# Kernel tuning notes

Hardware: AMD Instinct MI355X
Metric: run time of the kernel (lower is better)

The kernel has to match this reference:

```python
import jax, jax.numpy as jnp
import numpy as np

N = 50000      # nodes
IN = 128       # in_channels
H = 2          # heads
C = 64         # hidden_channels (per head)
E = 800000     # edges (before self-loops)
OUT = 40       # out_channels
BN_EPS = 1e-5
NEG_SLOPE = 0.2  # PyG GATConv default


def _bn(x, g, b):
    # BatchNorm1d forward with batch statistics (training-mode math, biased var)
    mu = jnp.mean(x, axis=0)
    v = jnp.var(x, axis=0)
    return (x - mu) * jax.lax.rsqrt(v + BN_EPS) * g + b


def _gat_conv(x, src, dst, W, a_src, a_dst, bias, concat):
    n = x.shape[0]
    h = (x @ W).reshape(n, H, C)                      # [N,H,C] per-head projection
    al_s = jnp.einsum('nhc,hc->nh', h, a_src)         # [N,H]
    al_d = jnp.einsum('nhc,hc->nh', h, a_dst)
    e = jax.nn.leaky_relu(al_s[src] + al_d[dst], NEG_SLOPE)  # [E,H]
    # segment softmax over edges sharing the same destination
    m = jax.ops.segment_max(e, dst, num_segments=n)
    ex = jnp.exp(e - m[dst])
    s = jax.ops.segment_sum(ex, dst, num_segments=n)
    alpha = ex / s[dst]                               # [E,H]
    out = jax.ops.segment_sum(h[src] * alpha[..., None], dst, num_segments=n)  # [N,H,C]
    out = out.reshape(n, H * C) if concat else out.mean(axis=1)
    return out + bias


def setup_inputs() -> dict:
    key = jax.random.key(0)
    ks = jax.random.split(key, 16)
    g = lambda k, shp, scale=1.0: jax.random.normal(k, shp, dtype=jnp.float32) * scale
    x = g(ks[0], (N, IN))
    edge_index = jax.random.randint(ks[1], (2, E), 0, N, dtype=jnp.int32)
    s = 1.0 / np.sqrt(IN)
    s2 = 1.0 / np.sqrt(H * C)
    return {
        'x': x,
        'edge_index': edge_index,
        'bn0_g': jnp.ones((IN,), jnp.float32), 'bn0_b': jnp.zeros((IN,), jnp.float32),
        'W1': g(ks[2], (IN, H * C), s), 'a1_src': g(ks[3], (H, C), s), 'a1_dst': g(ks[4], (H, C), s),
        'b1': jnp.zeros((H * C,), jnp.float32),
        'bn1_g': jnp.ones((H * C,), jnp.float32), 'bn1_b': jnp.zeros((H * C,), jnp.float32),
        'W2': g(ks[5], (H * C, H * C), s2), 'a2_src': g(ks[6], (H, C), s2), 'a2_dst': g(ks[7], (H, C), s2),
        'b2': jnp.zeros((C,), jnp.float32),
        'bn2_g': jnp.ones((C,), jnp.float32), 'bn2_b': jnp.zeros((C,), jnp.float32),
        'Wf': g(ks[8], (C, OUT), 1.0 / np.sqrt(C)), 'bf': jnp.zeros((OUT,), jnp.float32),
    }


def reference(x, edge_index, bn0_g, bn0_b, W1, a1_src, a1_dst, b1, bn1_g, bn1_b,
              W2, a2_src, a2_dst, b2, bn2_g, bn2_b, Wf, bf):
    n = x.shape[0]
    loop = jnp.arange(n, dtype=edge_index.dtype)
    src = jnp.concatenate([edge_index[0], loop])  # add self-loops (PyG default)
    dst = jnp.concatenate([edge_index[1], loop])
    h = _bn(x, bn0_g, bn0_b)
    # layer 1: concat heads
    h = _gat_conv(h, src, dst, W1, a1_src, a1_dst, b1, concat=True)
    h = jax.nn.elu(_bn(h, bn1_g, bn1_b))
    # (dropout is identity in eval mode)
    # layer 2: average heads
    h = _gat_conv(h, src, dst, W2, a2_src, a2_dst, b2, concat=False)
    h = jax.nn.elu(_bn(h, bn2_g, bn2_b))
    return h @ Wf + bf
```

## Files before the change

### kernel.cpp

```cpp
#include <hip/hip_runtime.h>
#include <hip/hip_fp16.h>


#define NEG_SLOPE 0.2f
#define BN_EPS 1e-5f

typedef short bf16x8 __attribute__((ext_vector_type(8)));
typedef float f32x4 __attribute__((ext_vector_type(4)));

static __device__ __forceinline__ unsigned short f2bf(float f) {
    union { float f; unsigned u; } v; v.f = f;
    unsigned r = v.u + 0x7FFF + ((v.u >> 16) & 1);
    return (unsigned short)(r >> 16);
}
static __device__ __forceinline__ float2 bf2x2(unsigned v) {
    union { unsigned u; float f; } a, b;
    a.u = v << 16; b.u = v & 0xffff0000u;
    return make_float2(a.f, b.f);
}
static __device__ __forceinline__ float halfsel(unsigned p, int head) {
    __half2 h = *(__half2*)&p;
    return head ? __high2float(h) : __low2float(h);
}

template <int C>
static __device__ __forceinline__ void d_bnstat(const float* __restrict__ x, int M,
                                                int rowsPerBlock, float* __restrict__ sums,
                                                int b) {
    constexpr int TPR = C / 4;
    constexpr int RS  = 256 / TPR;
    __shared__ float red[4][2 * C];
    const int t = threadIdx.x;
    const int cg = t % TPR, rg = t / TPR, w = t >> 6, lane = t & 63;
    int r0 = b * rowsPerBlock + rg;
    int r1 = min(M, b * rowsPerBlock + rowsPerBlock);
    float4 s = make_float4(0, 0, 0, 0), q = make_float4(0, 0, 0, 0);
    #pragma unroll 4
    for (int r = r0; r < r1; r += RS) {
        float4 v = *(const float4*)&x[(size_t)r * C + cg * 4];
        s.x += v.x; s.y += v.y; s.z += v.z; s.w += v.w;
        q.x += v.x * v.x; q.y += v.y * v.y; q.z += v.z * v.z; q.w += v.w * v.w;
    }
    #pragma unroll
    for (int off = TPR; off < 64; off <<= 1) {
        s.x += __shfl_xor(s.x, off); s.y += __shfl_xor(s.y, off);
        s.z += __shfl_xor(s.z, off); s.w += __shfl_xor(s.w, off);
        q.x += __shfl_xor(q.x, off); q.y += __shfl_xor(q.y, off);
        q.z += __shfl_xor(q.z, off); q.w += __shfl_xor(q.w, off);
    }
    if (lane < TPR) {
        *(float4*)&red[w][cg * 4] = s;
        *(float4*)&red[w][C + cg * 4] = q;
    }
    __syncthreads();
    for (int idx = t; idx < 2 * C; idx += 256) {
        float tot = red[0][idx] + red[1][idx] + red[2][idx] + red[3][idx];
        atomicAdd(&sums[idx], tot);
    }
}

template <int C>
__global__ __launch_bounds__(256) void k_bnstat2(const float* __restrict__ x, int M,
                                                 int rowsPerBlock, float* __restrict__ sums) {
    d_bnstat<C>(x, M, rowsPerBlock, sums, blockIdx.x);
}

__global__ __launch_bounds__(256) void k_prep(
    const int* __restrict__ ei, int E, int S, int NR,
    const float* __restrict__ x, int M, int bgrid,
    const float* __restrict__ W1, const float* __restrict__ W2,
    unsigned short* __restrict__ cnt, unsigned short* __restrict__ rank,
    float* __restrict__ sums,
    unsigned short* __restrict__ wt1, unsigned short* __restrict__ wt2) {
    int b = blockIdx.x;
    int CG = 8 * S;
    if (b < CG) {
        __shared__ unsigned lcnt[8192];
        const int t = threadIdx.x;
        const int r = b & 7, s = b >> 3;
        const unsigned lo = (unsigned)(r * NR);
        for (int j = t; j < NR; j += 256) lcnt[j] = 0;
        __syncthreads();
        int i1 = min(E, (s + 1) << 15);
        for (int i = (s << 15) + t; i < i1; i += 256) {
            unsigned d = (unsigned)ei[E + i];
            unsigned rel = d - lo;
            if (rel < (unsigned)NR) {
                unsigned old = atomicAdd(&lcnt[rel], 1u);
                rank[i] = (unsigned short)old;
            }
        }
        __syncthreads();
        for (int j = t; j < NR; j += 256) {
            int node = (int)lo + j;
            if (node < M) cnt[(size_t)s * M + node] = (unsigned short)lcnt[j];
        }
    } else if (b < CG + bgrid) {
        d_bnstat<128>(x, M, 256, sums, b - CG);
    } else {
        int idx = (b - CG - bgrid) * 256 + threadIdx.x;
        if (idx < 128 * 128) {
            int n = idx >> 7, k = idx & 127;
            wt1[idx] = f2bf(W1[k * 128 + n]);
            wt2[idx] = f2bf(W2[k * 128 + n]);
        }
    }
}

__global__ __launch_bounds__(1024) void k_part(const unsigned short* __restrict__ cnt,
                                               int Nn, int S, int* __restrict__ part) {
    __shared__ int ws[16];
    int t = threadIdx.x, lane = t & 63, w = t >> 6;
    int i = blockIdx.x * 1024 + t;
    int v = 0;
    if (i < Nn) {
        for (int s = 0; s < S; s++) v += (int)cnt[(size_t)s * Nn + i];
        v += 1;
    }
    #pragma unroll
    for (int off = 32; off; off >>= 1) v += __shfl_xor(v, off);
    if (lane == 0) ws[w] = v;
    __syncthreads();
    if (t < 16) {
        int s = ws[t];
        #pragma unroll
        for (int off = 8; off; off >>= 1) s += __shfl_xor(s, off);
        if (t == 0) part[blockIdx.x] = s;
    }
}

__global__ __launch_bounds__(1024) void k_scan2(unsigned short* __restrict__ cnt,
                                                int Nn, int S, int nb,
                                                const int* __restrict__ part,
                                                int* __restrict__ rowptr) {
    __shared__ int wsum[16];
    __shared__ int s_base, s_total;
    int t = threadIdx.x, lane = t & 63, w = t >> 6;
    int b = blockIdx.x;
    if (w == 0) {
        int base = 0, total = 0;
        for (int ch = 0; ch < nb; ch += 64) {
            int j = ch + lane;
            int v = (j < nb) ? part[j] : 0;
            total += v;
            base += (j < b) ? v : 0;
        }
        #pragma unroll
        for (int off = 32; off; off >>= 1) {
            base += __shfl_xor(base, off);
            total += __shfl_xor(total, off);
        }
        if (lane == 0) { s_base = base; s_total = total; }
    }
    int i = b * 1024 + t;
    int v = 0;
    if (i < Nn) {
        int run = 0;
        for (int s = 0; s < S; s++) {
            int cv = (int)cnt[(size_t)s * Nn + i];
            cnt[(size_t)s * Nn + i] = (unsigned short)run;
            run += cv;
        }
        v = run + 1;
    }
    int x = v;
    #pragma unroll
    for (int off = 1; off < 64; off <<= 1) {
        int y = __shfl_up(x, off);
        if (lane >= off) x += y;
    }
    if (lane == 63) wsum[w] = x;
    __syncthreads();
    if (w == 0) {
        int val = (lane < 16) ? wsum[lane] : 0;
        int xs = val;
        #pragma unroll
        for (int off = 1; off < 16; off <<= 1) {
            int y = __shfl_up(xs, off);
            if (lane >= off) xs += y;
        }
        if (lane < 16) wsum[lane] = xs - val;
    }
    __syncthreads();
    if (i < Nn) rowptr[i] = s_base + wsum[w] + (x - v);
    if (b == nb - 1 && t == 0) rowptr[Nn] = s_total;
}

static __device__ __forceinline__ void d_fill(int b, const int* __restrict__ ei,
                                              const unsigned short* __restrict__ rank,
                                              const unsigned short* __restrict__ pofs,
                                              const int* __restrict__ rowptr, int E, int Nn,
                                              unsigned short* __restrict__ ssrc) {
    int i = b * 256 + threadIdx.x;
    if (i < E) {
        int s = ei[i], d = ei[E + i];
        int p = i >> 15;
        int rk = (int)pofs[(size_t)p * Nn + d] + (int)rank[i];
        ssrc[rowptr[d] + 1 + rk] = (unsigned short)s;
    } else if (i < E + Nn) {
        int d = i - E;
        ssrc[rowptr[d]] = (unsigned short)d;
    }
}

static __device__ __forceinline__ void d_mfma(
    int blk, const float* __restrict__ A, const unsigned short* __restrict__ wt,
    const float* __restrict__ sums, const float* __restrict__ bng, const float* __restrict__ bnb,
    int elu, const float* __restrict__ asrc, const float* __restrict__ adst, int M,
    unsigned short* __restrict__ hb, float* __restrict__ als, float* __restrict__ ald) {
    __shared__ unsigned short As[64 * 136];
    __shared__ unsigned short Bs[128 * 136];
    __shared__ __align__(16) float stl[256];
    const int t = threadIdx.x;
    const int w = t >> 6, lane = t & 63;
    const int c = lane & 15, q = lane >> 4;
    const int row0 = blk * 64;

    if (t < 128) {
        float mu = sums[t] / (float)M;
        float var = sums[128 + t] / (float)M - mu * mu;
        float s = bng[t] * rsqrtf(var + BN_EPS);
        stl[t] = s;
        stl[128 + t] = bnb[t] - mu * s;
    }
    __syncthreads();

    #pragma unroll
    for (int i = 0; i < 8; i++) {
        int idx = t + i * 256;
        int r = idx >> 5, ch4 = idx & 31;
        int gr = row0 + r;
        float4 v = make_float4(0, 0, 0, 0);
        if (gr < M) {
            v = *(const float4*)&A[(size_t)gr * 128 + ch4 * 4];
            float4 sc = *(const float4*)&stl[ch4 * 4];
            float4 sh = *(const float4*)&stl[128 + ch4 * 4];
            v.x = v.x * sc.x + sh.x; v.y = v.y * sc.y + sh.y;
            v.z = v.z * sc.z + sh.z; v.w = v.w * sc.w + sh.w;
            if (elu) {
                v.x = v.x > 0.f ? v.x : expm1f(v.x);
                v.y = v.y > 0.f ? v.y : expm1f(v.y);
                v.z = v.z > 0.f ? v.z : expm1f(v.z);
                v.w = v.w > 0.f ? v.w : expm1f(v.w);
            }
        }
        unsigned p0 = ((unsigned)f2bf(v.y) << 16) | f2bf(v.x);
        unsigned p1 = ((unsigned)f2bf(v.w) << 16) | f2bf(v.z);
        *(uint2*)&As[r * 136 + ch4 * 4] = make_uint2(p0, p1);
    }
    #pragma unroll
    for (int i = 0; i < 8; i++) {
        int idx = t + i * 256;
        int r = idx >> 4, ch = idx & 15;
        *(uint4*)&Bs[r * 136 + ch * 8] = *(const uint4*)&wt[(size_t)r * 128 + ch * 8];
    }
    __syncthreads();

    f32x4 acc[8] = {};
    #pragma unroll
    for (int ks = 0; ks < 4; ks++) {
        bf16x8 a = *(bf16x8*)&As[(w * 16 + c) * 136 + (ks * 4 + q) * 8];
        #pragma unroll
        for (int tl = 0; tl < 8; tl++) {
            bf16x8 b = *(bf16x8*)&Bs[(tl * 16 + c) * 136 + (ks * 4 + q) * 8];
            acc[tl] = __builtin_amdgcn_mfma_f32_16x16x32_bf16(a, b, acc[tl], 0, 0, 0);
        }
    }

    #pragma unroll
    for (int reg = 0; reg < 4; reg++) {
        int grow = row0 + w * 16 + q * 4 + reg;
        if (grow < M) {
            #pragma unroll
            for (int tl = 0; tl < 8; tl++)
                hb[(size_t)grow * 128 + tl * 16 + c] = f2bf(acc[tl][reg]);
        }
    }

    float as_[8], ad_[8];
    #pragma unroll
    for (int tl = 0; tl < 8; tl++) { as_[tl] = asrc[tl * 16 + c]; ad_[tl] = adst[tl * 16 + c]; }
    #pragma unroll
    for (int reg = 0; reg < 4; reg++) {
        float s0 = 0.f, s1 = 0.f, d0 = 0.f, d1 = 0.f;
        #pragma unroll
        for (int tl = 0; tl < 4; tl++) { s0 += acc[tl][reg] * as_[tl]; d0 += acc[tl][reg] * ad_[tl]; }
        #pragma unroll
        for (int tl = 4; tl < 8; tl++) { s1 += acc[tl][reg] * as_[tl]; d1 += acc[tl][reg] * ad_[tl]; }
        #pragma unroll
        for (int off = 1; off < 16; off <<= 1) {
            s0 += __shfl_xor(s0, off); s1 += __shfl_xor(s1, off);
            d0 += __shfl_xor(d0, off); d1 += __shfl_xor(d1, off);
        }
        int grow = row0 + w * 16 + q * 4 + reg;
        if (c == 0 && grow < M) {
            *(float2*)&als[(size_t)grow * 2] = make_float2(s0, s1);
            *(float2*)&ald[(size_t)grow * 2] = make_float2(d0, d1);
        }
    }
}

__global__ __launch_bounds__(256) void k_mfma(
    const float* __restrict__ A, const unsigned short* __restrict__ wt,
    const float* __restrict__ sums, const float* __restrict__ bng, const float* __restrict__ bnb,
    int elu, const float* __restrict__ asrc, const float* __restrict__ adst, int M,
    unsigned short* __restrict__ hb, float* __restrict__ als, float* __restrict__ ald) {
    d_mfma(blockIdx.x, A, wt, sums, bng, bnb, elu, asrc, adst, M, hb, als, ald);
}

__global__ __launch_bounds__(256) void k_fill_mfma(
    const float* __restrict__ A, const unsigned short* __restrict__ wt,
    const float* __restrict__ sums, const float* __restrict__ bng, const float* __restrict__ bnb,
    const float* __restrict__ asrc, const float* __restrict__ adst, int M, int ggrid,
    unsigned short* __restrict__ hb, float* __restrict__ als, float* __restrict__ ald,
    const int* __restrict__ ei, const unsigned short* __restrict__ rank,
    const unsigned short* __restrict__ pofs,
    const int* __restrict__ rowptr, int E, int Nn, unsigned short* __restrict__ ssrc) {
    if (blockIdx.x < ggrid)
        d_mfma(blockIdx.x, A, wt, sums, bng, bnb, 0, asrc, adst, M, hb, als, ald);
    else
        d_fill(blockIdx.x - ggrid, ei, rank, pofs, rowptr, E, Nn, ssrc);
}

static __device__ __forceinline__ void acc8(float* acc, uint4 v, float a) {
    float2 p;
    p = bf2x2(v.x); acc[0] += a * p.x; acc[1] += a * p.y;
    p = bf2x2(v.y); acc[2] += a * p.x; acc[3] += a * p.y;
    p = bf2x2(v.z); acc[4] += a * p.x; acc[5] += a * p.y;
    p = bf2x2(v.w); acc[6] += a * p.x; acc[7] += a * p.y;
}

template <int MEAN>
static __device__ __forceinline__ void attnagg(
    const int* __restrict__ rowptr, const unsigned short* __restrict__ ssrc,
    const float* __restrict__ als, const float* __restrict__ ald,
    float* __restrict__ alpha, const unsigned short* __restrict__ hb,
    const float* __restrict__ bias, int Nn, float* __restrict__ out) {
    int gw = (blockIdx.x * blockDim.x + threadIdx.x) >> 6;
    if (gw >= Nn) return;
    int lane = threadIdx.x & 63;
    int sub = lane >> 4, c = lane & 15, head = c >> 3;
    int beg = rowptr[gw], end = rowptr[gw + 1];
    int deg = end - beg;
    float2 dv = *(const float2*)&ald[(size_t)gw * 2];
    float acc[8] = {};

    if (deg <= 64) {
        bool on = lane < deg;
        int eidx = beg + (on ? lane : 0);
        int sreg = (int)ssrc[eidx];
        float2 av = *(const float2*)&als[(size_t)sreg * 2];
        float v0 = av.x + dv.x; v0 = v0 > 0.f ? v0 : NEG_SLOPE * v0;
        float v1 = av.y + dv.y; v1 = v1 > 0.f ? v1 : NEG_SLOPE * v1;
        float p0 = on ? __expf(v0) : 0.f;
        float p1 = on ? __expf(v1) : 0.f;
        float t0 = p0, t1 = p1;
        #pragma unroll
        for (int off = 32; off; off >>= 1) {
            t0 += __shfl_xor(t0, off);
            t1 += __shfl_xor(t1, off);
        }
        __half2 hpk = __floats2half2_rn(p0 / t0, p1 / t1);
        unsigned pk = *(unsigned*)&hpk;

        int nit = (deg + 3) >> 2;
        int it = 0;
        for (; it + 4 <= nit; it += 4) {
            int s_[4]; float a_[4];
            #pragma unroll
            for (int u = 0; u < 4; u++) {
                int jj = (it + u) * 4 + sub;
                int ls = jj & 63;
                s_[u] = __shfl(sreg, ls);
                unsigned pw = (unsigned)__shfl(pk, ls);
                a_[u] = (jj < deg) ? halfsel(pw, head) : 0.f;
            }
            #pragma unroll
            for (int u = 0; u < 4; u++) {
                uint4 v = *(const uint4*)&hb[(size_t)s_[u] * 128 + c * 8];
                acc8(acc, v, a_[u]);
            }
        }
        for (; it < nit; it += 2) {
            const bool two = (it + 1) < nit;
            int s_[2]; float a_[2];
            #pragma unroll
            for (int u = 0; u < 2; u++) {
                if (u == 0 || two) {
                    int jj = (it + u) * 4 + sub;
                    int ls = jj & 63;
                    s_[u] = __shfl(sreg, ls);
                    unsigned pw = (unsigned)__shfl(pk, ls);
                    a_[u] = (jj < deg) ? halfsel(pw, head) : 0.f;
                }
            }
            #pragma unroll
            for (int u = 0; u < 2; u++) {
                if (u == 0 || two) {
                    uint4 v = *(const uint4*)&hb[(size_t)s_[u] * 128 + c * 8];
                    acc8(acc, v, a_[u]);
                }
            }
        }
    } else {
        float d0 = dv.x, d1 = dv.y;
        float m0 = -1e30f, m1 = -1e30f;
        for (int e = beg + lane; e < end; e += 64) {
            int s = (int)ssrc[e];
            float v0 = als[s * 2] + d0;     v0 = v0 > 0.f ? v0 : NEG_SLOPE * v0;
            float v1 = als[s * 2 + 1] + d1; v1 = v1 > 0.f ? v1 : NEG_SLOPE * v1;
            m0 = fmaxf(m0, v0); m1 = fmaxf(m1, v1);
        }
        #pragma unroll
        for (int off = 32; off; off >>= 1) {
            m0 = fmaxf(m0, __shfl_xor(m0, off));
            m1 = fmaxf(m1, __shfl_xor(m1, off));
        }
        float t0 = 0.f, t1 = 0.f;
        for (int e = beg + lane; e < end; e += 64) {
            int s = (int)ssrc[e];
            float v0 = als[s * 2] + d0;     v0 = v0 > 0.f ? v0 : NEG_SLOPE * v0;
            float v1 = als[s * 2 + 1] + d1; v1 = v1 > 0.f ? v1 : NEG_SLOPE * v1;
            float p0 = __expf(v0 - m0), p1 = __expf(v1 - m1);
            alpha[e * 2] = p0; alpha[e * 2 + 1] = p1;
            t0 += p0; t1 += p1;
        }
        #pragma unroll
        for (int off = 32; off; off >>= 1) {
            t0 += __shfl_xor(t0, off);
            t1 += __shfl_xor(t1, off);
        }
        float i0 = 1.f / t0, i1 = 1.f / t1;
        for (int e = beg + sub; e < end; e += 4) {
            int s = (int)ssrc[e];
            float a = (head ? alpha[(size_t)e * 2 + 1] * i1 : alpha[(size_t)e * 2] * i0);
            uint4 v = *(const uint4*)&hb[(size_t)s * 128 + c * 8];
            acc8(acc, v, a);
        }
    }

    #pragma unroll
    for (int j2 = 0; j2 < 8; j2++) {
        acc[j2] += __shfl_xor(acc[j2], 16);
        acc[j2] += __shfl_xor(acc[j2], 32);
        if (MEAN) acc[j2] += __shfl_xor(acc[j2], 8);
    }
    if (MEAN) {
        if (sub == 0 && c < 8) {
            float4 b0 = *(const float4*)&bias[c * 8];
            float4 b1 = *(const float4*)&bias[c * 8 + 4];
            float4 o0 = make_float4(0.5f * acc[0] + b0.x, 0.5f * acc[1] + b0.y, 0.5f * acc[2] + b0.z, 0.5f * acc[3] + b0.w);
            float4 o1 = make_float4(0.5f * acc[4] + b1.x, 0.5f * acc[5] + b1.y, 0.5f * acc[6] + b1.z, 0.5f * acc[7] + b1.w);
            *(float4*)&out[(size_t)gw * 64 + c * 8] = o0;
            *(float4*)&out[(size_t)gw * 64 + c * 8 + 4] = o1;
        }
    } else {
        if (sub == 0) {
            float4 b0 = *(const float4*)&bias[c * 8];
            float4 b1 = *(const float4*)&bias[c * 8 + 4];
            float4 o0 = make_float4(acc[0] + b0.x, acc[1] + b0.y, acc[2] + b0.z, acc[3] + b0.w);
            float4 o1 = make_float4(acc[4] + b1.x, acc[5] + b1.y, acc[6] + b1.z, acc[7] + b1.w);
            *(float4*)&out[(size_t)gw * 128 + c * 8] = o0;
            *(float4*)&out[(size_t)gw * 128 + c * 8 + 4] = o1;
        }
    }
}

__global__ __launch_bounds__(256) void k_attnagg1(const int* __restrict__ rowptr, const unsigned short* __restrict__ ssrc,
                                                  const float* __restrict__ als, const float* __restrict__ ald,
                                                  float* __restrict__ alpha, const unsigned short* __restrict__ hb,
                                                  const float* __restrict__ bias, int Nn, float* __restrict__ out) {
    attnagg<0>(rowptr, ssrc, als, ald, alpha, hb, bias, Nn, out);
}

__global__ __launch_bounds__(256) void k_attnagg2(const int* __restrict__ rowptr, const unsigned short* __restrict__ ssrc,
                                                  const float* __restrict__ als, const float* __restrict__ ald,
                                                  float* __restrict__ alpha, const unsigned short* __restrict__ hb,
                                                  const float* __restrict__ bias, int Nn, float* __restrict__ out) {
    attnagg<1>(rowptr, ssrc, als, ald, alpha, hb, bias, Nn, out);
}

__global__ __launch_bounds__(128) void k_gemmf(const float* __restrict__ A, const float* __restrict__ Wf,
                                               const float* __restrict__ bf,
                                               const float* __restrict__ sums, const float* __restrict__ bng,
                                               const float* __restrict__ bnb,
                                               int M, float* __restrict__ out) {
    __shared__ float As[128 * 65];
    __shared__ float Bs[64 * 40];
    __shared__ float stl[128];
    int t = threadIdx.x;
    int row0 = blockIdx.x * 128;
    if (t < 64) {
        float mu = sums[t] / (float)M;
        float var = sums[64 + t] / (float)M - mu * mu;
        float s = bng[t] * rsqrtf(var + BN_EPS);
        stl[t] = s;
        stl[64 + t] = bnb[t] - mu * s;
    }
    __syncthreads();
    for (int i = t; i < 64 * 40; i += 128) Bs[i] = Wf[i];
    for (int i = t; i < 128 * 64; i += 128) {
        int r = i >> 6, k = i & 63;
        int gr = row0 + r;
        float v = 0.f;
        if (gr < M) {
            v = A[(size_t)gr * 64 + k] * stl[k] + stl[64 + k];
            v = v > 0.f ? v : expm1f(v);
        }
        As[r * 65 + k] = v;
    }
    __syncthreads();
    int cg = t & 3, rg = t >> 2;
    float acc[4][10] = {};
    for (int k = 0; k < 64; k++) {
        float b[10];
        #pragma unroll
        for (int j = 0; j < 10; j++) b[j] = Bs[k * 40 + cg * 10 + j];
        #pragma unroll
        for (int r = 0; r < 4; r++) {
            float a = As[(rg * 4 + r) * 65 + k];
            #pragma unroll
            for (int j = 0; j < 10; j++) acc[r][j] += a * b[j];
        }
    }
    for (int r = 0; r < 4; r++) {
        int gr = row0 + rg * 4 + r;
        if (gr < M) {
            #pragma unroll
            for (int j = 0; j < 10; j++) out[(size_t)gr * 40 + cg * 10 + j] = acc[r][j] + bf[cg * 10 + j];
        }
    }
}

extern "C" void kernel_launch(void* const* d_in, const int* in_sizes, int n_in,
                              void* d_out, int out_size, void* d_ws, size_t ws_size,
                              hipStream_t stream) {
    const float* x     = (const float*)d_in[0];
    const int*   ei    = (const int*)d_in[1];
    const float* bn0_g = (const float*)d_in[2];
    const float* bn0_b = (const float*)d_in[3];
    const float* W1    = (const float*)d_in[4];
    const float* a1s   = (const float*)d_in[5];
    const float* a1d   = (const float*)d_in[6];
    const float* b1    = (const float*)d_in[7];
    const float* bn1_g = (const float*)d_in[8];
    const float* bn1_b = (const float*)d_in[9];
    const float* W2    = (const float*)d_in[10];
    const float* a2s   = (const float*)d_in[11];
    const float* a2d   = (const float*)d_in[12];
    const float* b2    = (const float*)d_in[13];
    const float* bn2_g = (const float*)d_in[14];
    const float* bn2_b = (const float*)d_in[15];
    const float* Wf    = (const float*)d_in[16];
    const float* bf    = (const float*)d_in[17];
    float* out = (float*)d_out;

    const int N  = in_sizes[0] / 128;
    const int E  = in_sizes[1] / 2;
    const int ET = E + N;
    const int S  = (E + 32767) >> 15;
    const int NR = (N + 7) / 8;

    char* ws = (char*)d_ws;
    size_t off = 0;
    auto alloc = [&](size_t bytes) -> char* {
        char* p = ws + off;
        off = (off + bytes + 255) & ~(size_t)255;
        return p;
    };
    float* sums   = (float*)alloc(640 * 4);
    const size_t zlen = off;
    unsigned short* cnt = (unsigned short*)alloc((size_t)S * N * 2);
    int*   rowptr = (int*)alloc((size_t)(N + 1) * 4);
    unsigned short* ssrc = (unsigned short*)alloc((size_t)ET * 2);
    unsigned short* rank = (unsigned short*)alloc((size_t)E * 2);
    float* abuf   = (float*)alloc((size_t)N * 128 * 4);
    unsigned short* hb  = (unsigned short*)alloc((size_t)N * 128 * 2);
    unsigned short* wt1 = (unsigned short*)alloc((size_t)128 * 128 * 2);
    unsigned short* wt2 = (unsigned short*)alloc((size_t)128 * 128 * 2);
    float* alpha  = (float*)alloc((size_t)ET * 2 * 4);
    float* als    = (float*)alloc((size_t)N * 2 * 4);
    float* ald    = (float*)alloc((size_t)N * 2 * 4);
    int*   part   = (int*)alloc(1024 * 4);

    const int tb = 256;
    const int CG = 8 * S;
    const int bgrid = (N + 255) / 256;
    const int fgrid = (ET + tb - 1) / tb;
    const int wgrid = ((size_t)N * 64 + tb - 1) / tb;
    const int ggrid = (N + 63) / 64;
    const int nscan = (N + 1023) / 1024;

    hipMemsetAsync(ws, 0, zlen, stream);

    k_prep<<<CG + bgrid + 64, tb, 0, stream>>>(ei, E, S, NR, x, N, bgrid, W1, W2,
                                               cnt, rank, sums, wt1, wt2);
    k_part<<<nscan, 1024, 0, stream>>>(cnt, N, S, part);
    k_scan2<<<nscan, 1024, 0, stream>>>(cnt, N, S, nscan, part, rowptr);

    k_fill_mfma<<<ggrid + fgrid, tb, 0, stream>>>(x, wt1, sums, bn0_g, bn0_b,
                                                  a1s, a1d, N, ggrid, hb, als, ald,
                                                  ei, rank, cnt, rowptr, E, N, ssrc);
    k_attnagg1<<<wgrid, tb, 0, stream>>>(rowptr, ssrc, als, ald, alpha, hb, b1, N, abuf);

    k_bnstat2<128><<<bgrid, 256, 0, stream>>>(abuf, N, 256, sums + 256);

    k_mfma<<<ggrid, tb, 0, stream>>>(abuf, wt2, sums + 256, bn1_g, bn1_b, 1, a2s, a2d, N, hb, als, ald);
    k_attnagg2<<<wgrid, tb, 0, stream>>>(rowptr, ssrc, als, ald, alpha, hb, b2, N, abuf);

    k_bnstat2<64><<<bgrid, 256, 0, stream>>>(abuf, N, 256, sums + 512);

    k_gemmf<<<(N + 127) / 128, 128, 0, stream>>>(abuf, Wf, bf, sums + 512, bn2_g, bn2_b, N, out);
}
```

Baseline: 330.4 us.

## Pack per-node counters as 16-bit pairs and shrink edge chunks for counting

The edge counting stage now packs two 16-bit node counters into each 32-bit shared word. This halves shared memory per block, and a shared buffer is reused between the counting and BN-stat paths, which should allow higher occupancy. Edge chunks shrink from 32768 to 8192 edges, which quadruples the number of counting blocks to spread the work across more CUs. In exchange, the per-chunk count array grows fourfold, which makes the later partition, scan and fill kernels read more count data.

New measurement: 332.8 us. No clear change (+0.7%).

```diff
diff --git a/kernel.cpp b/kernel.cpp
--- a/kernel.cpp
+++ b/kernel.cpp
@@ -4,6 +4,8 @@
 
 #define NEG_SLOPE 0.2f
 #define BN_EPS 1e-5f
+#define SH 13
+#define NRANGE 8
 
 typedef short bf16x8 __attribute__((ext_vector_type(8)));
 typedef float f32x4 __attribute__((ext_vector_type(4)));
@@ -26,10 +28,9 @@
 template <int C>
 static __device__ __forceinline__ void d_bnstat(const float* __restrict__ x, int M,
                                                 int rowsPerBlock, float* __restrict__ sums,
-                                                int b) {
+                                                int b, float* red) {
     constexpr int TPR = C / 4;
     constexpr int RS  = 256 / TPR;
-    __shared__ float red[4][2 * C];
     const int t = threadIdx.x;
     const int cg = t % TPR, rg = t / TPR, w = t >> 6, lane = t & 63;
     int r0 = b * rowsPerBlock + rg;
@@ -49,12 +50,12 @@
         q.z += __shfl_xor(q.z, off); q.w += __shfl_xor(q.w, off);
     }
     if (lane < TPR) {
-        *(float4*)&red[w][cg * 4] = s;
-        *(float4*)&red[w][C + cg * 4] = q;
+        *(float4*)&red[w * 2 * C + cg * 4] = s;
+        *(float4*)&red[w * 2 * C + C + cg * 4] = q;
     }
     __syncthreads();
     for (int idx = t; idx < 2 * C; idx += 256) {
-        float tot = red[0][idx] + red[1][idx] + red[2][idx] + red[3][idx];
+        float tot = red[idx] + red[2 * C + idx] + red[4 * C + idx] + red[6 * C + idx];
         atomicAdd(&sums[idx], tot);
     }
 }
@@ -62,7 +63,8 @@
 template <int C>
 __global__ __launch_bounds__(256) void k_bnstat2(const float* __restrict__ x, int M,
                                                  int rowsPerBlock, float* __restrict__ sums) {
-    d_bnstat<C>(x, M, rowsPerBlock, sums, blockIdx.x);
+    __shared__ __align__(16) float red[4 * 2 * C];
+    d_bnstat<C>(x, M, rowsPerBlock, sums, blockIdx.x, red);
 }
 
 __global__ __launch_bounds__(256) void k_prep(
@@ -72,31 +74,36 @@
     unsigned short* __restrict__ cnt, unsigned short* __restrict__ rank,
     float* __restrict__ sums,
     unsigned short* __restrict__ wt1, unsigned short* __restrict__ wt2) {
+    __shared__ __align__(16) unsigned smem[3200];
     int b = blockIdx.x;
-    int CG = 8 * S;
+    int CG = NRANGE * S;
     if (b < CG) {
-        __shared__ unsigned lcnt[8192];
+        unsigned* lcnt = smem;
         const int t = threadIdx.x;
         const int r = b & 7, s = b >> 3;
         const unsigned lo = (unsigned)(r * NR);
-        for (int j = t; j < NR; j += 256) lcnt[j] = 0;
+        const int NRW = NR >> 1;
+        for (int j = t; j < NRW; j += 256) lcnt[j] = 0;
         __syncthreads();
-        int i1 = min(E, (s + 1) << 15);
-        for (int i = (s << 15) + t; i < i1; i += 256) {
+        int i1 = min(E, (s + 1) << SH);
+        #pragma unroll 4
+        for (int i = (s << SH) + t; i < i1; i += 256) {
             unsigned d = (unsigned)ei[E + i];
             unsigned rel = d - lo;
             if (rel < (unsigned)NR) {
-                unsigned old = atomicAdd(&lcnt[rel], 1u);
-                rank[i] = (unsigned short)old;
+                unsigned sh = (rel & 1) << 4;
+                unsigned old = atomicAdd(&lcnt[rel >> 1], 1u << sh);
+                rank[i] = (unsigned short)((old >> sh) & 0xffffu);
             }
         }
         __syncthreads();
-        for (int j = t; j < NR; j += 256) {
-            int node = (int)lo + j;
-            if (node < M) cnt[(size_t)s * M + node] = (unsigned short)lcnt[j];
+        for (int j = t; j < NRW; j += 256) {
+            int node = (int)lo + 2 * j;
+            if (node < M)
+                *(unsigned*)&cnt[(size_t)s * M + node] = lcnt[j];
         }
     } else if (b < CG + bgrid) {
-        d_bnstat<128>(x, M, 256, sums, b - CG);
+        d_bnstat<128>(x, M, 256, sums, b - CG, (float*)smem);
     } else {
         int idx = (b - CG - bgrid) * 256 + threadIdx.x;
         if (idx < 128 * 128) {
@@ -194,7 +201,7 @@
     int i = b * 256 + threadIdx.x;
     if (i < E) {
         int s = ei[i], d = ei[E + i];
-        int p = i >> 15;
+        int p = i >> SH;
         int rk = (int)pofs[(size_t)p * Nn + d] + (int)rank[i];
         ssrc[rowptr[d] + 1 + rk] = (unsigned short)s;
     } else if (i < E + Nn) {
@@ -558,8 +565,8 @@
     const int N  = in_sizes[0] / 128;
     const int E  = in_sizes[1] / 2;
     const int ET = E + N;
-    const int S  = (E + 32767) >> 15;
-    const int NR = (N + 7) / 8;
+    const int S  = (E + (1 << SH) - 1) >> SH;
+    const int NR = (((N + NRANGE - 1) / NRANGE) + 1) & ~1;
 
     char* ws = (char*)d_ws;
     size_t off = 0;
@@ -584,7 +591,7 @@
     int*   part   = (int*)alloc(1024 * 4);
 
     const int tb = 256;
-    const int CG = 8 * S;
+    const int CG = NRANGE * S;
     const int bgrid = (N + 255) / 256;
     const int fgrid = (ET + tb - 1) / tb;
     const int wgrid = ((size_t)N * 64 + tb - 1) / tb;
```
